# Optimization experiments

Measured on AMD Instinct MI355X. Metric: run time of the kernel, lower is better.

The kernel has to match this reference:

```python
import jax, jax.numpy as jnp
import numpy as np

K = 3
PAD = 1
DIL = 1
STRIDE = 1


def _conv(x, w, b):
    y = jax.lax.conv_general_dilated(
        x, w, (STRIDE, STRIDE), [(PAD, PAD), (PAD, PAD)],
        rhs_dilation=(DIL, DIL),
        dimension_numbers=("NCHW", "OIHW", "NCHW"))
    return y + b[None, :, None, None]


def setup_inputs() -> dict:
    key = jax.random.key(0)
    ks = jax.random.split(key, 6)
    B, C, H, W = 4, 64, 128, 128
    O = 64
    x = jax.random.normal(ks[0], (B, C, H, W), dtype=jnp.float32)
    # original zero-inits offset/mod convs; use small random weights so offsets are nontrivial
    w_off = jax.random.normal(ks[1], (2 * K * K, C, K, K), dtype=jnp.float32) * 0.02
    b_off = jnp.zeros((2 * K * K,), dtype=jnp.float32)
    w_mod = jax.random.normal(ks[2], (K * K, C, K, K), dtype=jnp.float32) * 0.02
    b_mod = jnp.zeros((K * K,), dtype=jnp.float32)
    w_reg = jax.random.normal(ks[3], (O, C, K, K), dtype=jnp.float32) * (1.0 / np.sqrt(C * K * K))
    return {"x": x, "w_off": w_off, "b_off": b_off, "w_mod": w_mod, "b_mod": b_mod, "w_reg": w_reg}


def _deform_conv(x, offset, mask, w_reg):
    B, C, H, W = x.shape
    Ho, Wo = offset.shape[2], offset.shape[3]
    KK = K * K
    # torchvision layout: channel 2*k = dy, 2*k+1 = dx, k = i*K+j
    off = offset.reshape(B, KK, 2, Ho, Wo)
    dy, dx = off[:, :, 0], off[:, :, 1]          # (B,KK,Ho,Wo)
    ky, kx = jnp.meshgrid(jnp.arange(K), jnp.arange(K), indexing="ij")
    base_y = (jnp.arange(Ho) * STRIDE - PAD)[None, :, None] + (ky.reshape(-1) * DIL)[:, None, None]
    base_x = (jnp.arange(Wo) * STRIDE - PAD)[None, None, :] + (kx.reshape(-1) * DIL)[:, None, None]
    py = dy + base_y[None].astype(x.dtype)       # (B,KK,Ho,Wo) sampling rows
    px = dx + base_x[None].astype(x.dtype)       # (B,KK,Ho,Wo) sampling cols

    y0f = jnp.floor(py)
    x0f = jnp.floor(px)
    wy = py - y0f
    wx = px - x0f
    y0 = y0f.astype(jnp.int32)
    x0 = x0f.astype(jnp.int32)

    xf = x.reshape(B, C, H * W)

    def gather(iy, ix):
        valid = ((iy >= 0) & (iy < H) & (ix >= 0) & (ix < W)).astype(x.dtype)
        idx = jnp.clip(iy, 0, H - 1) * W + jnp.clip(ix, 0, W - 1)   # (B,KK,Ho,Wo)
        v = jax.vmap(lambda xb, ib: xb[:, ib])(xf, idx.reshape(B, -1))  # (B,C,KK*Ho*Wo)
        return v.reshape(B, C, KK, Ho, Wo) * valid[:, None]

    wy_ = wy[:, None]
    wx_ = wx[:, None]
    samp = (gather(y0, x0) * (1 - wy_) * (1 - wx_)
            + gather(y0, x0 + 1) * (1 - wy_) * wx_
            + gather(y0 + 1, x0) * wy_ * (1 - wx_)
            + gather(y0 + 1, x0 + 1) * wy_ * wx_)
    samp = samp * mask[:, None]                   # modulated im2col (B,C,KK,Ho,Wo)
    O = w_reg.shape[0]
    return jnp.einsum("bckhw,ock->bohw", samp, w_reg.reshape(O, C, KK))


def reference(x, w_off, b_off, w_mod, b_mod, w_reg):
    offset = _conv(x, w_off, b_off)                       # (B, 2*K*K, Ho, Wo)
    mask = 2.0 * jax.nn.sigmoid(_conv(x, w_mod, b_mod))    # (B, K*K, Ho, Wo)
    return _deform_conv(x, offset, mask, w_reg)
```

## Files before the change

kernel.cpp:

```cpp
#include <hip/hip_runtime.h>
#include <math.h>

#define BDIM 256
#define TP   32
#define C_   64
#define O_   64
#define H_   128
#define W_   128
#define KK_  9
#define CKK  576
#define HW_  (H_ * W_)
#define XTP  72
#define XCOLS 34
#define NE   (TP * KK_)
#define NBLK 2048
#define SROW 584

#define WTAB_OFF  131072
#define ITAB_OFF  (WTAB_OFF + (size_t)NBLK * NE * 16)
#define XHBF_OFF  (ITAB_OFF + (size_t)NBLK * NE * 8)
#define WS_NEED   (XHBF_OFF + (size_t)4 * HW_ * C_ * 2)

typedef short short8 __attribute__((ext_vector_type(8)));
typedef float f32x4  __attribute__((ext_vector_type(4)));

__device__ __forceinline__ unsigned short f2bf(float f) {
    unsigned int u = __float_as_uint(f);
    u += 0x7FFFu + ((u >> 16) & 1u);
    return (unsigned short)(u >> 16);
}

__device__ __forceinline__ unsigned int pk2bf(float lo, float hi) {
    unsigned int r;
    asm("v_cvt_pk_bf16_f32 %0, %1, %2" : "=v"(r) : "v"(lo), "v"(hi));
    return r;
}

__device__ __forceinline__ float bf_lo(unsigned int u) { return __uint_as_float(u << 16); }
__device__ __forceinline__ float bf_hi(unsigned int u) { return __uint_as_float(u & 0xFFFF0000u); }

__global__ __launch_bounds__(BDIM) void dcn_pre(
    const float* __restrict__ x,
    unsigned short* __restrict__ xhbf,
    const float* __restrict__ w_off, const float* __restrict__ w_mod,
    const float* __restrict__ w_reg, unsigned short* __restrict__ wpack)
{
    __shared__ float tile[32][33];
    if (blockIdx.x >= 4096) {
        int i = (blockIdx.x - 4096) * BDIM + threadIdx.x;
        bool isB = i < 36864;
        int r = isB ? i : i - 36864;
        int j    = r & 7;
        int lane = (r >> 3) & 63;
        int t2   = r >> 9;
        int kstep = t2 % 18;
        int tilei = t2 / 18;
        int k  = kstep * 32 + (lane >> 4) * 8 + j;
        int c  = k & 63;
        int kk = k >> 6;
        int col = tilei * 16 + (lane & 15);
        float v;
        if (isB) {
            v = w_reg[(size_t)col * CKK + c * KK_ + kk];
        } else {
            if (col < 18)      v = w_off[(size_t)col * CKK + c * KK_ + kk];
            else if (col < 27) v = w_mod[(size_t)(col - 18) * CKK + c * KK_ + kk];
            else               v = 0.f;
        }
        wpack[i] = f2bf(v);
        return;
    }
    int wq = blockIdx.x & 3;
    int cq = (blockIdx.x >> 2) & 1;
    int by = blockIdx.x >> 3;
    int b = by >> 7, y = by & 127;
    int w0 = wq * 32, c0 = cq * 32;
    int tw = threadIdx.x & 31, tc = threadIdx.x >> 5;
    const float* xp = x + (size_t)b * C_ * HW_ + (size_t)y * W_;
    #pragma unroll
    for (int k = 0; k < 4; ++k)
        tile[tc + k * 8][tw] = xp[(size_t)(c0 + tc + k * 8) * HW_ + w0 + tw];
    __syncthreads();
    unsigned int* opb = (unsigned int*)xhbf + ((size_t)b * HW_ + (size_t)y * W_) * 32;
    for (int u = threadIdx.x; u < 512; u += BDIM) {
        int wp = u >> 4;
        int cp = u & 15;
        opb[(size_t)(w0 + wp) * 32 + (c0 >> 1) + cp] =
            pk2bf(tile[2 * cp][wp], tile[2 * cp + 1][wp]);
    }
}

__global__ __launch_bounds__(BDIM, 4) void dcn_tabs(
    const unsigned short* __restrict__ xhbf,
    const float* __restrict__ b_off,
    const float* __restrict__ b_mod,
    const unsigned short* __restrict__ wO,
    float4* __restrict__ wtab_g,
    ushort4* __restrict__ itab_g)
{
    __shared__ __align__(16) unsigned short xtile[102 * XTP];
    __shared__ float offs[TP * 18];
    __shared__ float msk [TP * KK_];

    const int t    = threadIdx.x;
    const int wave = t >> 6;
    const int lane = t & 63;
    const int blk  = ((blockIdx.x & 7) << 8) | (blockIdx.x >> 3);
    const int wo0  = (blk & 3) * TP;
    const int ho   = (blk >> 2) & 127;
    const int b    = blk >> 9;

    const unsigned short* xbh = xhbf + (size_t)b * HW_ * C_;

    for (int u = t; u < 102 * 8; u += BDIM) {
        int row = u >> 3;
        int c8  = (u & 7) * 8;
        int ry  = row / XCOLS;
        int col = row - ry * XCOLS;
        int gy  = ho - 1 + ry;
        int gx  = wo0 - 1 + col;
        uint4 v = make_uint4(0u, 0u, 0u, 0u);
        if (gy >= 0 && gy < H_ && gx >= 0 && gx < W_)
            v = *(const uint4*)&xbh[((size_t)(gy * W_ + gx) << 6) + c8];
        *(uint4*)&xtile[row * XTP + c8] = v;
    }
    __syncthreads();

    if (wave < 2) {
        f32x4 acc0 = {0.f, 0.f, 0.f, 0.f};
        f32x4 acc1 = {0.f, 0.f, 0.f, 0.f};
        const unsigned short* bp = wO + ((size_t)(wave * 18) * 64 + lane) * 8;
        const unsigned short* ap = xtile + (lane & 15) * XTP + (lane >> 4) * 8;
        #pragma unroll
        for (int ks = 0; ks < 18; ++ks) {
            const int kk = ks >> 1, ky = kk / 3, kx = kk - ky * 3;
            const int ro = (ky * XCOLS + kx) * XTP + (ks & 1) * 32;
            short8 av0 = *(const short8*)&ap[ro];
            short8 av1 = *(const short8*)&ap[ro + 16 * XTP];
            short8 bv  = *(const short8*)bp;  bp += 512;
            acc0 = __builtin_amdgcn_mfma_f32_16x16x32_bf16(av0, bv, acc0, 0, 0, 0);
            acc1 = __builtin_amdgcn_mfma_f32_16x16x32_bf16(av1, bv, acc1, 0, 0, 0);
        }
        int oc   = wave * 16 + (lane & 15);
        int prow = (lane >> 4) * 4;
        if (oc < 18) {
            float bias = b_off[oc];
            #pragma unroll
            for (int r = 0; r < 4; ++r) {
                offs[(prow + r) * 18 + oc]      = acc0[r] + bias;
                offs[(prow + 16 + r) * 18 + oc] = acc1[r] + bias;
            }
        } else if (oc < 27) {
            int mc = oc - 18;
            float bias = b_mod[mc];
            #pragma unroll
            for (int r = 0; r < 4; ++r) {
                msk[(prow + r) * KK_ + mc]      = 2.f / (1.f + expf(-(acc0[r] + bias)));
                msk[(prow + 16 + r) * KK_ + mc] = 2.f / (1.f + expf(-(acc1[r] + bias)));
            }
        }
    }
    __syncthreads();

    float4*  wg = wtab_g + (size_t)blk * NE;
    ushort4* ig = itab_g + (size_t)blk * NE;
    for (int e = t; e < NE; e += BDIM) {
        int p  = e / 9;
        int kk = e - p * 9;
        int ky = kk / 3, kx = kk - ky * 3;
        float dy = offs[p * 18 + 2 * kk];
        float dx = offs[p * 18 + 2 * kk + 1];
        float py = dy + (float)(ho - 1 + ky);
        float px = dx + (float)(wo0 + p - 1 + kx);
        float y0f = floorf(py), x0f = floorf(px);
        float wy = py - y0f,    wx = px - x0f;
        int y0 = (int)y0f, x0 = (int)x0f;
        int y1 = y0 + 1,   x1 = x0 + 1;
        float m = msk[p * KK_ + kk];
        float vy0 = (y0 >= 0 && y0 < H_) ? 1.f : 0.f;
        float vy1 = (y1 >= 0 && y1 < H_) ? 1.f : 0.f;
        float vx0 = (x0 >= 0 && x0 < W_) ? 1.f : 0.f;
        float vx1 = (x1 >= 0 && x1 < W_) ? 1.f : 0.f;
        float4 wt;
        wt.x = (1.f - wy) * (1.f - wx) * m * vy0 * vx0;
        wt.y = (1.f - wy) * wx * m * vy0 * vx1;
        wt.z = wy * (1.f - wx) * m * vy1 * vx0;
        wt.w = wy * wx * m * vy1 * vx1;
        int yc0 = min(max(y0, 0), H_ - 1), yc1 = min(max(y1, 0), H_ - 1);
        int xc0 = min(max(x0, 0), W_ - 1), xc1 = min(max(x1, 0), W_ - 1);
        wg[e] = wt;
        ig[e] = make_ushort4((unsigned short)(yc0 * W_ + xc0),
                             (unsigned short)(yc0 * W_ + xc1),
                             (unsigned short)(yc1 * W_ + xc0),
                             (unsigned short)(yc1 * W_ + xc1));
    }
}

__global__ __launch_bounds__(BDIM, 4) void dcn_gather(
    const unsigned short* __restrict__ xhbf,
    const float4* __restrict__ wtab_g,
    const ushort4* __restrict__ itab_g,
    const unsigned short* __restrict__ wB,
    float* __restrict__ out)
{
    __shared__ __align__(16) unsigned short samp_s[TP * SROW];

    const int t    = threadIdx.x;
    const int wave = t >> 6;
    const int lane = t & 63;
    const int blk  = ((blockIdx.x & 7) << 8) | (blockIdx.x >> 3);
    const int wo0  = (blk & 3) * TP;
    const int ho   = (blk >> 2) & 127;
    const int b    = blk >> 9;

    const unsigned short* xbh = xhbf + (size_t)b * HW_ * C_;

    {
        const int c8 = (lane & 7) * 8;
        const int q  = lane >> 3;
        const int e0 = wave * 72 + q;
        const unsigned short* base = xbh + c8;
        const float4*  wg = wtab_g + (size_t)blk * NE;
        const ushort4* ig = itab_g + (size_t)blk * NE;

        ushort4 ixr[9];
        float4  wtr[9];
        #pragma unroll
        for (int it = 0; it < 9; ++it) {
            ixr[it] = ig[e0 + it * 8];
            wtr[it] = wg[e0 + it * 8];
        }

        #pragma unroll
        for (int it = 0; it < 9; ++it) {
            const int e  = e0 + it * 8;
            const int p  = (e * 29128) >> 18;
            const int kk = e - p * 9;
            const int dst = p * SROW + kk * 64;
            float4  wt = wtr[it];
            ushort4 ix = ixr[it];
            uint4 u00 = *(const uint4*)(base + ((size_t)ix.x << 6));
            uint4 u01 = *(const uint4*)(base + ((size_t)ix.y << 6));
            uint4 u10 = *(const uint4*)(base + ((size_t)ix.z << 6));
            uint4 u11 = *(const uint4*)(base + ((size_t)ix.w << 6));
            const unsigned int a00[4] = {u00.x, u00.y, u00.z, u00.w};
            const unsigned int a01[4] = {u01.x, u01.y, u01.z, u01.w};
            const unsigned int a10[4] = {u10.x, u10.y, u10.z, u10.w};
            const unsigned int a11[4] = {u11.x, u11.y, u11.z, u11.w};
            unsigned int pk[4];
            #pragma unroll
            for (int wd = 0; wd < 4; ++wd) {
                float slo = bf_lo(a00[wd]) * wt.x;
                slo = fmaf(bf_lo(a01[wd]), wt.y, slo);
                slo = fmaf(bf_lo(a10[wd]), wt.z, slo);
                slo = fmaf(bf_lo(a11[wd]), wt.w, slo);
                float shi = bf_hi(a00[wd]) * wt.x;
                shi = fmaf(bf_hi(a01[wd]), wt.y, shi);
                shi = fmaf(bf_hi(a10[wd]), wt.z, shi);
                shi = fmaf(bf_hi(a11[wd]), wt.w, shi);
                pk[wd] = pk2bf(slo, shi);
            }
            *(uint4*)&samp_s[dst + c8] = make_uint4(pk[0], pk[1], pk[2], pk[3]);
        }
    }
    __syncthreads();

    {
        f32x4 acc0 = {0.f, 0.f, 0.f, 0.f};
        f32x4 acc1 = {0.f, 0.f, 0.f, 0.f};
        const unsigned short* bp = wB + ((size_t)(wave * 18) * 64 + lane) * 8;
        const int arow = (lane & 15) * SROW + (lane >> 4) * 8;
        #pragma unroll
        for (int ks = 0; ks < 18; ++ks) {
            const int ro = arow + (ks >> 1) * 64 + (ks & 1) * 32;
            short8 av0 = *(const short8*)&samp_s[ro];
            short8 av1 = *(const short8*)&samp_s[ro + 16 * SROW];
            short8 bv  = *(const short8*)bp;  bp += 512;
            acc0 = __builtin_amdgcn_mfma_f32_16x16x32_bf16(av0, bv, acc0, 0, 0, 0);
            acc1 = __builtin_amdgcn_mfma_f32_16x16x32_bf16(av1, bv, acc1, 0, 0, 0);
        }
        int o    = wave * 16 + (lane & 15);
        int prow = (lane >> 4) * 4;
        float* ob = out + (size_t)b * O_ * HW_ + (size_t)o * HW_ + ho * W_ + wo0;
        #pragma unroll
        for (int r = 0; r < 4; ++r) {
            ob[prow + r]      = acc0[r];
            ob[16 + prow + r] = acc1[r];
        }
    }
}

extern "C" void kernel_launch(void* const* d_in, const int* in_sizes, int n_in,
                              void* d_out, int out_size, void* d_ws, size_t ws_size,
                              hipStream_t stream) {
    const float* x     = (const float*)d_in[0];
    const float* w_off = (const float*)d_in[1];
    const float* b_off = (const float*)d_in[2];
    const float* w_mod = (const float*)d_in[3];
    const float* b_mod = (const float*)d_in[4];
    const float* w_reg = (const float*)d_in[5];
    float* out = (float*)d_out;

    unsigned short* wpack = (unsigned short*)d_ws;
    float4*  wtab_g = (float4*)((char*)d_ws + WTAB_OFF);
    ushort4* itab_g = (ushort4*)((char*)d_ws + ITAB_OFF);
    unsigned short* x_hbf = (unsigned short*)((char*)d_ws + XHBF_OFF);

    dcn_pre<<<4096 + 216, BDIM, 0, stream>>>(x, x_hbf, w_off, w_mod, w_reg, wpack);
    dcn_tabs<<<NBLK, BDIM, 0, stream>>>(x_hbf, b_off, b_mod,
                                        wpack + 36864, wtab_g, itab_g);
    dcn_gather<<<NBLK, BDIM, 0, stream>>>(x_hbf, wtab_g, itab_g, wpack, out);
}
```

Baseline: 43.42 us.

## Fuse offset/mask table kernel into gather kernel via shared-memory tables

Merges the offset/mask convolution kernel and the bilinear gather+GEMM kernel into one kernel. Sampling weights and indices now live in LDS instead of a global workspace. The offset-conv input tile and the offs/msk arrays reuse the samp_s buffer. This removes a kernel launch and the global write and read of the tables. In exchange, LDS per block grows and launch bounds drop from 4 to 3 blocks per CU, which may reduce occupancy and latency hiding.

```diff
diff --git a/kernel.cpp b/kernel.cpp
--- a/kernel.cpp
+++ b/kernel.cpp
@@ -16,9 +16,7 @@
 #define NBLK 2048
 #define SROW 584
 
-#define WTAB_OFF  131072
-#define ITAB_OFF  (WTAB_OFF + (size_t)NBLK * NE * 16)
-#define XHBF_OFF  (ITAB_OFF + (size_t)NBLK * NE * 8)
+#define XHBF_OFF  131072
 #define WS_NEED   (XHBF_OFF + (size_t)4 * HW_ * C_ * 2)
 
 typedef short short8 __attribute__((ext_vector_type(8)));
@@ -90,17 +88,20 @@
     }
 }
 
-__global__ __launch_bounds__(BDIM, 4) void dcn_tabs(
+__global__ __launch_bounds__(BDIM, 3) void dcn_main(
     const unsigned short* __restrict__ xhbf,
     const float* __restrict__ b_off,
     const float* __restrict__ b_mod,
+    const unsigned short* __restrict__ wB,
     const unsigned short* __restrict__ wO,
-    float4* __restrict__ wtab_g,
-    ushort4* __restrict__ itab_g)
+    float* __restrict__ out)
 {
-    __shared__ __align__(16) unsigned short xtile[102 * XTP];
-    __shared__ float offs[TP * 18];
-    __shared__ float msk [TP * KK_];
+    __shared__ __align__(16) unsigned short samp_s[TP * SROW];
+    __shared__ __align__(16) float4 wtab[NE];
+    __shared__ ushort4        itab[NE];
+
+    float* offs = (float*)(samp_s + 8192);
+    float* msk  = offs + TP * 18;
 
     const int t    = threadIdx.x;
     const int wave = t >> 6;
@@ -122,7 +123,7 @@
         uint4 v = make_uint4(0u, 0u, 0u, 0u);
         if (gy >= 0 && gy < H_ && gx >= 0 && gx < W_)
             v = *(const uint4*)&xbh[((size_t)(gy * W_ + gx) << 6) + c8];
-        *(uint4*)&xtile[row * XTP + c8] = v;
+        *(uint4*)&samp_s[row * XTP + c8] = v;
     }
     __syncthreads();
 
@@ -130,7 +131,7 @@
         f32x4 acc0 = {0.f, 0.f, 0.f, 0.f};
         f32x4 acc1 = {0.f, 0.f, 0.f, 0.f};
         const unsigned short* bp = wO + ((size_t)(wave * 18) * 64 + lane) * 8;
-        const unsigned short* ap = xtile + (lane & 15) * XTP + (lane >> 4) * 8;
+        const unsigned short* ap = samp_s + (lane & 15) * XTP + (lane >> 4) * 8;
         #pragma unroll
         for (int ks = 0; ks < 18; ++ks) {
             const int kk = ks >> 1, ky = kk / 3, kx = kk - ky * 3;
@@ -162,8 +163,6 @@
     }
     __syncthreads();
 
-    float4*  wg = wtab_g + (size_t)blk * NE;
-    ushort4* ig = itab_g + (size_t)blk * NE;
     for (int e = t; e < NE; e += BDIM) {
         int p  = e / 9;
         int kk = e - p * 9;
@@ -188,47 +187,26 @@
         wt.w = wy * wx * m * vy1 * vx1;
         int yc0 = min(max(y0, 0), H_ - 1), yc1 = min(max(y1, 0), H_ - 1);
         int xc0 = min(max(x0, 0), W_ - 1), xc1 = min(max(x1, 0), W_ - 1);
-        wg[e] = wt;
-        ig[e] = make_ushort4((unsigned short)(yc0 * W_ + xc0),
-                             (unsigned short)(yc0 * W_ + xc1),
-                             (unsigned short)(yc1 * W_ + xc0),
-                             (unsigned short)(yc1 * W_ + xc1));
-    }
-}
-
-__global__ __launch_bounds__(BDIM, 4) void dcn_gather(
-    const unsigned short* __restrict__ xhbf,
-    const float4* __restrict__ wtab_g,
-    const ushort4* __restrict__ itab_g,
-    const unsigned short* __restrict__ wB,
-    float* __restrict__ out)
-{
-    __shared__ __align__(16) unsigned short samp_s[TP * SROW];
-
-    const int t    = threadIdx.x;
-    const int wave = t >> 6;
-    const int lane = t & 63;
-    const int blk  = ((blockIdx.x & 7) << 8) | (blockIdx.x >> 3);
-    const int wo0  = (blk & 3) * TP;
-    const int ho   = (blk >> 2) & 127;
-    const int b    = blk >> 9;
-
-    const unsigned short* xbh = xhbf + (size_t)b * HW_ * C_;
+        wtab[e] = wt;
+        itab[e] = make_ushort4((unsigned short)(yc0 * W_ + xc0),
+                               (unsigned short)(yc0 * W_ + xc1),
+                               (unsigned short)(yc1 * W_ + xc0),
+                               (unsigned short)(yc1 * W_ + xc1));
+    }
+    __syncthreads();
 
     {
         const int c8 = (lane & 7) * 8;
         const int q  = lane >> 3;
         const int e0 = wave * 72 + q;
         const unsigned short* base = xbh + c8;
-        const float4*  wg = wtab_g + (size_t)blk * NE;
-        const ushort4* ig = itab_g + (size_t)blk * NE;
 
         ushort4 ixr[9];
         float4  wtr[9];
         #pragma unroll
         for (int it = 0; it < 9; ++it) {
-            ixr[it] = ig[e0 + it * 8];
-            wtr[it] = wg[e0 + it * 8];
+            ixr[it] = itab[e0 + it * 8];
+            wtr[it] = wtab[e0 + it * 8];
         }
 
         #pragma unroll
@@ -302,12 +280,9 @@
     float* out = (float*)d_out;
 
     unsigned short* wpack = (unsigned short*)d_ws;
-    float4*  wtab_g = (float4*)((char*)d_ws + WTAB_OFF);
-    ushort4* itab_g = (ushort4*)((char*)d_ws + ITAB_OFF);
     unsigned short* x_hbf = (unsigned short*)((char*)d_ws + XHBF_OFF);
 
     dcn_pre<<<4096 + 216, BDIM, 0, stream>>>(x, x_hbf, w_off, w_mod, w_reg, wpack);
-    dcn_tabs<<<NBLK, BDIM, 0, stream>>>(x_hbf, b_off, b_mod,
-                                        wpack + 36864, wtab_g, itab_g);
-    dcn_gather<<<NBLK, BDIM, 0, stream>>>(x_hbf, wtab_g, itab_g, wpack, out);
-}
+    dcn_main<<<NBLK, BDIM, 0, stream>>>(x_hbf, b_off, b_mod,
+                                        wpack, wpack + 36864, out);
+}
```

After: 44.87 us. +3.4%, slower.
